# Optimization experiments

Measured on AMD Instinct MI355X. Metric: run time of the kernel, lower is better.

The kernel has to match this reference:

```python
import jax, jax.numpy as jnp
import numpy as np

NUM_HEADS = 16
EPS = 1e-5
BLOCK = 16  # score_mod: q_idx // 16 == kv_idx % 16


def _ln(x, eps=EPS):
    # LayerNorm, elementwise_affine=False
    m = jnp.mean(x, axis=-1, keepdims=True)
    v = jnp.mean((x - m) ** 2, axis=-1, keepdims=True)
    return (x - m) * jax.lax.rsqrt(v + eps)


def setup_inputs() -> dict:
    key = jax.random.key(0)
    ks = jax.random.split(key, 5)
    N, D = 2048, 2048
    w = 0.02
    return {
        "x": jax.random.normal(ks[0], (N, D), jnp.float32),
        "Wq": jax.random.normal(ks[1], (D, D), jnp.float32) * w,
        "Wk": jax.random.normal(ks[2], (D, D), jnp.float32) * w,
        "Wv": jax.random.normal(ks[3], (D, D), jnp.float32) * w,
        "Wo": jax.random.normal(ks[4], (D, D), jnp.float32) * w,
    }


def reference(x, Wq, Wk, Wv, Wo):
    N, D = x.shape
    H = NUM_HEADS
    DH = D // H
    x_in = x
    xn = _ln(x)
    # per-head q/k layernorm, cast to attention dtype (bfloat16)
    q = _ln((xn @ Wq).reshape(N, H, DH)).astype(jnp.bfloat16)
    k = _ln((xn @ Wk).reshape(N, H, DH)).astype(jnp.bfloat16)
    v = (xn @ Wv).reshape(N, H, DH)  # stays fp32 (original applies no cast to vs)
    scale = 1.0 / np.sqrt(DH)
    # dense scores then sparsity mask, as flex_attention with score_mod does
    scores = jnp.einsum("nhd,mhd->hnm", q, k, preferred_element_type=jnp.float32) * scale
    qi = jnp.arange(N)
    mask = (qi[:, None] // BLOCK) == (qi[None, :] % BLOCK)  # [N, N]
    s = jnp.where(mask[None, :, :], scores, -jnp.inf)
    # safe softmax: rows with no allowed keys (q_idx >= 256) produce zeros
    mx = jnp.max(s, axis=-1, keepdims=True)
    e = jnp.exp(s - jnp.where(jnp.isfinite(mx), mx, 0.0))
    denom = jnp.sum(e, axis=-1, keepdims=True)
    attn = e / jnp.maximum(denom, 1e-30)
    o = jnp.einsum("hnm,mhd->nhd", attn, v)  # [N, H, DH]
    out = o.reshape(N, D) @ Wo
    return out + x_in
```

## Files before the change

kernel.cpp:

```cpp
#include <hip/hip_runtime.h>

typedef unsigned short u16;
typedef __attribute__((ext_vector_type(8))) short short8;
typedef __attribute__((ext_vector_type(4))) float f32x4;

#define D 2048
#define EPS 1e-5f

__device__ __forceinline__ u16 f2bf(float f) {
  unsigned u = __float_as_uint(f);
  u += 0x7fffu + ((u >> 16) & 1u);
  return (u16)(u >> 16);
}

__device__ __forceinline__ void async16(const void* g, void* l) {
  __builtin_amdgcn_global_load_lds(
      (const __attribute__((address_space(1))) void*)g,
      (__attribute__((address_space(3))) void*)l, 16, 0, 0);
}

__global__ __launch_bounds__(256) void prep(const float* __restrict__ x,
                                            const float* __restrict__ Wq,
                                            const float* __restrict__ Wk,
                                            const float* __restrict__ Wv,
                                            const float* __restrict__ Wo,
                                            u16* __restrict__ xn,
                                            float* __restrict__ out,
                                            u16* __restrict__ WqT, u16* __restrict__ WkT,
                                            u16* __restrict__ WvT, u16* __restrict__ WoT) {
  int bid = blockIdx.x;
  int t = threadIdx.x;
  if (bid < 2048) {
    const float* xr = x + (size_t)bid * D;
    float4 v[2];
    float s = 0.f, sq = 0.f;
#pragma unroll
    for (int i = 0; i < 2; i++) {
      v[i] = *(const float4*)(xr + i * 1024 + t * 4);
      s += v[i].x + v[i].y + v[i].z + v[i].w;
      sq += v[i].x * v[i].x + v[i].y * v[i].y + v[i].z * v[i].z + v[i].w * v[i].w;
    }
#pragma unroll
    for (int m = 32; m >= 1; m >>= 1) { s += __shfl_xor(s, m); sq += __shfl_xor(sq, m); }
    __shared__ float ps[4], pq[4];
    int w = t >> 6, lane = t & 63;
    if (lane == 0) { ps[w] = s; pq[w] = sq; }
    __syncthreads();
    s = ps[0] + ps[1] + ps[2] + ps[3];
    sq = pq[0] + pq[1] + pq[2] + pq[3];
    float mean = s * (1.f / D);
    float var = sq * (1.f / D) - mean * mean;
    float rs = rsqrtf(var + EPS);
    float* outr = out + (size_t)bid * D;
    u16* xnr = xn + (size_t)bid * D;
#pragma unroll
    for (int i = 0; i < 2; i++) {
      *(float4*)(outr + i * 1024 + t * 4) = v[i];
      ushort4 o;
      o.x = f2bf((v[i].x - mean) * rs);
      o.y = f2bf((v[i].y - mean) * rs);
      o.z = f2bf((v[i].z - mean) * rs);
      o.w = f2bf((v[i].w - mean) * rs);
      *(ushort4*)(xnr + i * 1024 + t * 4) = o;
    }
  } else {
    int tb = bid - 2048;
    int wsel = tb >> 10;
    int tt = tb & 1023;
    const float* src; u16* dst;
    switch (wsel) {
      case 0: src = Wq; dst = WqT; break;
      case 1: src = Wk; dst = WkT; break;
      case 2: src = Wv; dst = WvT; break;
      default: src = Wo; dst = WoT; break;
    }
    int i0 = (tt >> 5) * 64, j0 = (tt & 31) * 64;
    __shared__ u16 tile[64 * 66];
#pragma unroll
    for (int r = 0; r < 4; r++) {
      int idx = r * 256 + t;
      int row = idx >> 4, c4 = idx & 15;
      float4 v = *(const float4*)(src + (size_t)(i0 + row) * D + j0 + c4 * 4);
      tile[row * 66 + c4 * 4 + 0] = f2bf(v.x);
      tile[row * 66 + c4 * 4 + 1] = f2bf(v.y);
      tile[row * 66 + c4 * 4 + 2] = f2bf(v.z);
      tile[row * 66 + c4 * 4 + 3] = f2bf(v.w);
    }
    __syncthreads();
#pragma unroll
    for (int r = 0; r < 4; r++) {
      int idx = r * 256 + t;
      int row = idx >> 4, c4 = idx & 15;
      ushort4 o;
      o.x = tile[(c4 * 4 + 0) * 66 + row];
      o.y = tile[(c4 * 4 + 1) * 66 + row];
      o.z = tile[(c4 * 4 + 2) * 66 + row];
      o.w = tile[(c4 * 4 + 3) * 66 + row];
      *(ushort4*)(dst + (size_t)(j0 + row) * D + i0 + c4 * 4) = o;
    }
  }
}

__device__ __forceinline__ void gemm_tile(const u16* __restrict__ A,
                                          const u16* __restrict__ Bt,
                                          bool permB, int m0, int n0,
                                          int kbeg, int kend,
                                          u16* As, u16* Bs, f32x4 acc[4][4]) {
  int tid = threadIdx.x, wid = tid >> 6, lane = tid & 63;
  int q4 = lane >> 4, m16 = lane & 15;
  int wm = wid >> 1, wn = wid & 1;
  for (int kb = kbeg; kb < kend; kb += 64) {
#pragma unroll
    for (int p = 0; p < 4; p++) {
      int idx = p * 256 + tid;
      int r = idx >> 3, sl = idx & 7;
      int gc = sl ^ (r & 7);
      async16(A + (size_t)(m0 + r) * D + kb + gc * 8, As + (size_t)(p * 256 + wid * 64) * 8);
      int rb = n0 + r;
      int gr = permB ? ((rb & 127) * 16 + (rb >> 7)) : rb;
      async16(Bt + (size_t)gr * D + kb + gc * 8, Bs + (size_t)(p * 256 + wid * 64) * 8);
    }
    __syncthreads();
#pragma unroll
    for (int ks = 0; ks < 2; ks++) {
      short8 af[4], bf[4];
      int c = ks * 4 + q4;
#pragma unroll
      for (int i = 0; i < 4; i++) {
        int ra = wm * 64 + i * 16 + m16;
        af[i] = *(const short8*)(As + ra * 64 + (c ^ (ra & 7)) * 8);
        int rb = wn * 64 + i * 16 + m16;
        bf[i] = *(const short8*)(Bs + rb * 64 + (c ^ (rb & 7)) * 8);
      }
#pragma unroll
      for (int i = 0; i < 4; i++)
#pragma unroll
        for (int j = 0; j < 4; j++)
          acc[i][j] = __builtin_amdgcn_mfma_f32_16x16x32_bf16(af[i], bf[j], acc[i][j], 0, 0, 0);
    }
    __syncthreads();
  }
}

__global__ __launch_bounds__(256, 3) void gemm_mega(const u16* __restrict__ xn,
                                                    const u16* __restrict__ WkT,
                                                    const u16* __restrict__ WvT,
                                                    const u16* __restrict__ WqT,
                                                    u16* __restrict__ K3,
                                                    u16* __restrict__ V3,
                                                    float* __restrict__ Qp) {
  __shared__ u16 smem[2 * 128 * 64];
  u16* As = smem;
  u16* Bs = smem + 8192;
  int bid0 = blockIdx.x;
  int tid = threadIdx.x, wid = tid >> 6, lane = tid & 63;
  int q4 = lane >> 4, m16 = lane & 15;
  int wm = wid >> 1, wn = wid & 1;

  if (bid0 >= 512) {
    int qb = bid0 - 512;
    int ks = qb & 7, t = qb >> 3;
    int m0 = (t >> 4) * 128, n0 = (t & 15) * 128;
    f32x4 acc[4][4];
#pragma unroll
    for (int i = 0; i < 4; i++)
#pragma unroll
      for (int j = 0; j < 4; j++)
#pragma unroll
        for (int r = 0; r < 4; r++) acc[i][j][r] = 0.f;
    gemm_tile(xn, WqT, false, m0, n0, ks * 256, ks * 256 + 256, As, Bs, acc);
    float* C = Qp + (size_t)ks * 256 * D;
#pragma unroll
    for (int i = 0; i < 4; i++)
#pragma unroll
      for (int j = 0; j < 4; j++)
#pragma unroll
        for (int r = 0; r < 4; r++) {
          int row = m0 + wm * 64 + i * 16 + q4 * 4 + r;
          int col = n0 + wn * 64 + j * 16 + m16;
          C[(size_t)row * D + col] = acc[i][j][r];
        }
    return;
  }

  int bid = (bid0 & 7) * 64 + (bid0 >> 3);
  int sel = bid >> 8;
  int z = bid & 255;
  int m0 = (z >> 4) * 128, n0 = (z & 15) * 128;
  const u16* A = sel ? WvT : xn;
  const u16* Bt = sel ? xn : WkT;
  f32x4 acc[4][4];
#pragma unroll
  for (int i = 0; i < 4; i++)
#pragma unroll
    for (int j = 0; j < 4; j++)
#pragma unroll
      for (int r = 0; r < 4; r++) acc[i][j][r] = 0.f;
  gemm_tile(A, Bt, sel == 1, m0, n0, 0, D, As, Bs, acc);

  if (sel == 1) {
    int h = m0 >> 7, b = n0 >> 7;
#pragma unroll
    for (int i = 0; i < 4; i++)
#pragma unroll
      for (int j = 0; j < 4; j++)
#pragma unroll
        for (int r = 0; r < 4; r++) {
          int dhl = wm * 64 + i * 16 + q4 * 4 + r;
          int key = wn * 64 + j * 16 + m16;
          V3[((size_t)(h * 16 + b) * 128 + dhl) * 128 + key] = f2bf(acc[i][j][r]);
        }
  } else {
    float* redS = (float*)smem;
    float* redQ = redS + 256;
    __syncthreads();
#pragma unroll
    for (int i = 0; i < 4; i++) {
      float ps[4], pq[4];
#pragma unroll
      for (int r = 0; r < 4; r++) {
        float s = 0.f, q = 0.f;
#pragma unroll
        for (int j = 0; j < 4; j++) { float a = acc[i][j][r]; s += a; q += a * a; }
#pragma unroll
        for (int msk = 1; msk < 16; msk <<= 1) {
          s += __shfl_xor(s, msk);
          q += __shfl_xor(q, msk);
        }
        ps[r] = s; pq[r] = q;
      }
      if (m16 == 0) {
#pragma unroll
        for (int r = 0; r < 4; r++) {
          int row = wm * 64 + i * 16 + q4 * 4 + r;
          redS[row * 2 + wn] = ps[r];
          redQ[row * 2 + wn] = pq[r];
        }
      }
    }
    __syncthreads();
    int h = n0 >> 7;
#pragma unroll
    for (int i = 0; i < 4; i++)
#pragma unroll
      for (int r = 0; r < 4; r++) {
        int row = wm * 64 + i * 16 + q4 * 4 + r;
        float S = redS[row * 2] + redS[row * 2 + 1];
        float Qs = redQ[row * 2] + redQ[row * 2 + 1];
        float mean = S * (1.f / 128.f);
        float var = Qs * (1.f / 128.f) - mean * mean;
        float rstd = rsqrtf(var + EPS);
        int tok = m0 + row;
#pragma unroll
        for (int j = 0; j < 4; j++) {
          int dhl = wn * 64 + j * 16 + m16;
          u16 val = f2bf((acc[i][j][r] - mean) * rstd);
          K3[(((size_t)(h * 16 + (tok & 15))) * 128 + (tok >> 4)) * 128 + dhl] = val;
        }
      }
  }
}

__global__ __launch_bounds__(256) void attn(const float* __restrict__ Qp,
                                            const u16* __restrict__ K3,
                                            const u16* __restrict__ V3,
                                            u16* __restrict__ Ob) {
  int bh = blockIdx.x;
  int h = bh & 15, b = bh >> 4;
  int tid = threadIdx.x, w = tid >> 6, lane = tid & 63;
  int q4 = lane >> 4, m16 = lane & 15;
  __shared__ u16 Qs[16][136];
  __shared__ u16 P[16][136];
  __shared__ float redmx[4][16];
  __shared__ float redsm[4][16];
  __shared__ float invd[16];
  const float scale = 0.08838834764831845f;
  const u16* Ktile = K3 + (size_t)(h * 16 + b) * 128 * 128;
  const u16* Vtile = V3 + (size_t)(h * 16 + b) * 128 * 128;

  {
    int row = tid >> 4;
    int c8 = (tid & 15) * 8;
    const float* qpb = Qp + (size_t)(b * 16 + row) * D + h * 128 + c8;
    float q8[8];
#pragma unroll
    for (int ii = 0; ii < 8; ii++) q8[ii] = 0.f;
#pragma unroll
    for (int ks = 0; ks < 8; ks++) {
      float4 a = *(const float4*)(qpb + (size_t)ks * 256 * D);
      float4 bb = *(const float4*)(qpb + (size_t)ks * 256 * D + 4);
      q8[0] += a.x; q8[1] += a.y; q8[2] += a.z; q8[3] += a.w;
      q8[4] += bb.x; q8[5] += bb.y; q8[6] += bb.z; q8[7] += bb.w;
    }
    float s = 0.f, sq = 0.f;
#pragma unroll
    for (int ii = 0; ii < 8; ii++) { s += q8[ii]; sq += q8[ii] * q8[ii]; }
#pragma unroll
    for (int msk = 1; msk < 16; msk <<= 1) { s += __shfl_xor(s, msk); sq += __shfl_xor(sq, msk); }
    float mean = s * (1.f / 128.f);
    float var = sq * (1.f / 128.f) - mean * mean;
    float rstd = rsqrtf(var + EPS);
#pragma unroll
    for (int ii = 0; ii < 8; ii++) Qs[row][c8 + ii] = f2bf((q8[ii] - mean) * rstd);
  }
  __syncthreads();

  short8 af[4];
#pragma unroll
  for (int dc = 0; dc < 4; dc++)
    af[dc] = *(const short8*)(&Qs[m16][dc * 32 + q4 * 8]);
  f32x4 s[2];
#pragma unroll
  for (int kt = 0; kt < 2; kt++)
#pragma unroll
    for (int r = 0; r < 4; r++) s[kt][r] = 0.f;
#pragma unroll
  for (int kt = 0; kt < 2; kt++) {
    int key = w * 32 + kt * 16 + m16;
#pragma unroll
    for (int dc = 0; dc < 4; dc++) {
      short8 bf = *(const short8*)(Ktile + (size_t)key * 128 + dc * 32 + q4 * 8);
      s[kt] = __builtin_amdgcn_mfma_f32_16x16x32_bf16(af[dc], bf, s[kt], 0, 0, 0);
    }
  }
  float mx[4];
#pragma unroll
  for (int r = 0; r < 4; r++) {
    mx[r] = fmaxf(s[0][r], s[1][r]);
#pragma unroll
    for (int msk = 1; msk < 16; msk <<= 1) mx[r] = fmaxf(mx[r], __shfl_xor(mx[r], msk));
    if (m16 == 0) redmx[w][q4 * 4 + r] = mx[r];
  }
  __syncthreads();
#pragma unroll
  for (int r = 0; r < 4; r++) {
    int row = q4 * 4 + r;
    float M = fmaxf(fmaxf(redmx[0][row], redmx[1][row]), fmaxf(redmx[2][row], redmx[3][row]));
    float acc = 0.f;
#pragma unroll
    for (int kt = 0; kt < 2; kt++) {
      float e = __expf((s[kt][r] - M) * scale);
      s[kt][r] = e;
      acc += e;
    }
#pragma unroll
    for (int msk = 1; msk < 16; msk <<= 1) acc += __shfl_xor(acc, msk);
    if (m16 == 0) redsm[w][row] = acc;
  }
#pragma unroll
  for (int kt = 0; kt < 2; kt++)
#pragma unroll
    for (int r = 0; r < 4; r++)
      P[q4 * 4 + r][w * 32 + kt * 16 + m16] = f2bf(s[kt][r]);
  __syncthreads();
  if (tid < 16) invd[tid] = 1.0f / (redsm[0][tid] + redsm[1][tid] + redsm[2][tid] + redsm[3][tid]);
  __syncthreads();

  short8 pf[4];
#pragma unroll
  for (int kc = 0; kc < 4; kc++)
    pf[kc] = *(const short8*)(&P[m16][kc * 32 + q4 * 8]);
  f32x4 o[2];
#pragma unroll
  for (int dt = 0; dt < 2; dt++)
#pragma unroll
    for (int r = 0; r < 4; r++) o[dt][r] = 0.f;
#pragma unroll
  for (int dt = 0; dt < 2; dt++) {
    int dhl = w * 32 + dt * 16 + m16;
#pragma unroll
    for (int kc = 0; kc < 4; kc++) {
      short8 vf = *(const short8*)(Vtile + (size_t)dhl * 128 + kc * 32 + q4 * 8);
      o[dt] = __builtin_amdgcn_mfma_f32_16x16x32_bf16(pf[kc], vf, o[dt], 0, 0, 0);
    }
  }
#pragma unroll
  for (int dt = 0; dt < 2; dt++)
#pragma unroll
    for (int r = 0; r < 4; r++) {
      int row = q4 * 4 + r;
      float val = o[dt][r] * invd[row];
      Ob[(size_t)(b * 16 + row) * D + h * 128 + w * 32 + dt * 16 + m16] = f2bf(val);
    }
}

__global__ __launch_bounds__(256, 3) void gemm_wo(const u16* __restrict__ Ob,
                                                  const u16* __restrict__ WoT,
                                                  float* __restrict__ Wpart) {
  __shared__ u16 smem[2 * 128 * 64];
  u16* As = smem;
  u16* Bs = smem + 8192;
  int m0 = blockIdx.x * 128, n0 = blockIdx.y * 128;
  int z = blockIdx.z;
  int k0 = z * 256;
  f32x4 acc[4][4];
#pragma unroll
  for (int i = 0; i < 4; i++)
#pragma unroll
    for (int j = 0; j < 4; j++)
#pragma unroll
      for (int r = 0; r < 4; r++) acc[i][j][r] = 0.f;
  gemm_tile(Ob, WoT, false, m0, n0, k0, k0 + 256, As, Bs, acc);
  float* C = Wpart + (size_t)z * 256 * D;
  int tid = threadIdx.x, wid = tid >> 6, lane = tid & 63;
  int q4 = lane >> 4, m16 = lane & 15;
  int wm = wid >> 1, wn = wid & 1;
#pragma unroll
  for (int i = 0; i < 4; i++)
#pragma unroll
    for (int j = 0; j < 4; j++)
#pragma unroll
      for (int r = 0; r < 4; r++) {
        int row = m0 + wm * 64 + i * 16 + q4 * 4 + r;
        int col = n0 + wn * 64 + j * 16 + m16;
        C[(size_t)row * D + col] = acc[i][j][r];
      }
}

__global__ __launch_bounds__(256) void reduce_wo(const float* __restrict__ Wpart,
                                                 float* __restrict__ out) {
  int i = (blockIdx.x * 256 + threadIdx.x) * 4;
  float4 s = *(const float4*)(out + i);
#pragma unroll
  for (int z = 0; z < 8; z++) {
    float4 p = *(const float4*)(Wpart + (size_t)z * 256 * D + i);
    s.x += p.x; s.y += p.y; s.z += p.z; s.w += p.w;
  }
  *(float4*)(out + i) = s;
}

extern "C" void kernel_launch(void* const* d_in, const int* in_sizes, int n_in,
                              void* d_out, int out_size, void* d_ws, size_t ws_size,
                              hipStream_t stream) {
  const float* x  = (const float*)d_in[0];
  const float* Wq = (const float*)d_in[1];
  const float* Wk = (const float*)d_in[2];
  const float* Wv = (const float*)d_in[3];
  const float* Wo = (const float*)d_in[4];
  float* out = (float*)d_out;
  char* w = (char*)d_ws;
  const size_t MB = 1u << 20;
  u16*   xn    = (u16*)(w);
  u16*   WqT   = (u16*)(w + 8 * MB);
  u16*   WkT   = (u16*)(w + 16 * MB);
  u16*   WvT   = (u16*)(w + 24 * MB);
  u16*   WoT   = (u16*)(w + 32 * MB);
  u16*   K3    = (u16*)(w + 40 * MB);
  u16*   V3    = (u16*)(w + 48 * MB);
  u16*   Obf   = (u16*)(w + 56 * MB);
  float* Qp    = (float*)(w + 58 * MB);
  float* Wpart = (float*)(w + 58 * MB);

  prep<<<dim3(6144), dim3(256), 0, stream>>>(x, Wq, Wk, Wv, Wo, xn, out, WqT, WkT, WvT, WoT);
  gemm_mega<<<dim3(768), dim3(256), 0, stream>>>(xn, WkT, WvT, WqT, K3, V3, Qp);
  attn<<<dim3(256), dim3(256), 0, stream>>>(Qp, K3, V3, Obf);
  gemm_wo<<<dim3(2, 16, 8), dim3(256), 0, stream>>>(Obf, WoT, Wpart);
  reduce_wo<<<dim3(512), dim3(256), 0, stream>>>(Wpart, out);
}
```

Measured before the change: 191.5 us.

## Fuse attention, Wo GEMM and reduction into one persistent kernel with grid barriers

Merges the attn, gemm_wo and reduce_wo launches into a single 256-block kernel, using atomic-counter grid barriers between phases. The barrier counters are reset inside the prep kernel. The aim is to remove two kernel launch gaps and their tail effects. In exchange, correctness depends on all 256 blocks being co-resident, the spin barriers add cost, and Qp and Wpart share workspace memory across phases that are now inside one kernel.

```diff
diff --git a/kernel.cpp b/kernel.cpp
--- a/kernel.cpp
+++ b/kernel.cpp
@@ -17,6 +17,18 @@
   __builtin_amdgcn_global_load_lds(
       (const __attribute__((address_space(1))) void*)g,
       (__attribute__((address_space(3))) void*)l, 16, 0, 0);
+}
+
+__device__ __forceinline__ void gridbar(unsigned* ctr) {
+  __syncthreads();
+  if (threadIdx.x == 0) {
+    __threadfence();
+    __hip_atomic_fetch_add(ctr, 1u, __ATOMIC_ACQ_REL, __HIP_MEMORY_SCOPE_AGENT);
+    while (__hip_atomic_load(ctr, __ATOMIC_ACQUIRE, __HIP_MEMORY_SCOPE_AGENT) < 256u)
+      __builtin_amdgcn_s_sleep(2);
+  }
+  __syncthreads();
+  __threadfence();
 }
 
 __global__ __launch_bounds__(256) void prep(const float* __restrict__ x,
@@ -27,9 +39,11 @@
                                             u16* __restrict__ xn,
                                             float* __restrict__ out,
                                             u16* __restrict__ WqT, u16* __restrict__ WkT,
-                                            u16* __restrict__ WvT, u16* __restrict__ WoT) {
+                                            u16* __restrict__ WvT, u16* __restrict__ WoT,
+                                            unsigned* __restrict__ bar) {
   int bid = blockIdx.x;
   int t = threadIdx.x;
+  if (bid == 2048 && t < 2) bar[t] = 0;
   if (bid < 2048) {
     const float* xr = x + (size_t)bid * D;
     float4 v[2];
@@ -261,172 +275,184 @@
   }
 }
 
-__global__ __launch_bounds__(256) void attn(const float* __restrict__ Qp,
-                                            const u16* __restrict__ K3,
-                                            const u16* __restrict__ V3,
-                                            u16* __restrict__ Ob) {
-  int bh = blockIdx.x;
-  int h = bh & 15, b = bh >> 4;
+__global__ __launch_bounds__(256, 2) void tail(const float* __restrict__ Qp,
+                                               const u16* __restrict__ K3,
+                                               const u16* __restrict__ V3,
+                                               const u16* __restrict__ WoT,
+                                               float* __restrict__ Wpart,
+                                               float* __restrict__ out,
+                                               u16* __restrict__ Ob,
+                                               unsigned* __restrict__ bar) {
+  __shared__ u16 smem[2 * 128 * 64];
+  int bid = blockIdx.x;
   int tid = threadIdx.x, w = tid >> 6, lane = tid & 63;
   int q4 = lane >> 4, m16 = lane & 15;
-  __shared__ u16 Qs[16][136];
-  __shared__ u16 P[16][136];
-  __shared__ float redmx[4][16];
-  __shared__ float redsm[4][16];
-  __shared__ float invd[16];
-  const float scale = 0.08838834764831845f;
-  const u16* Ktile = K3 + (size_t)(h * 16 + b) * 128 * 128;
-  const u16* Vtile = V3 + (size_t)(h * 16 + b) * 128 * 128;
 
   {
-    int row = tid >> 4;
-    int c8 = (tid & 15) * 8;
-    const float* qpb = Qp + (size_t)(b * 16 + row) * D + h * 128 + c8;
-    float q8[8];
-#pragma unroll
-    for (int ii = 0; ii < 8; ii++) q8[ii] = 0.f;
-#pragma unroll
-    for (int ks = 0; ks < 8; ks++) {
-      float4 a = *(const float4*)(qpb + (size_t)ks * 256 * D);
-      float4 bb = *(const float4*)(qpb + (size_t)ks * 256 * D + 4);
-      q8[0] += a.x; q8[1] += a.y; q8[2] += a.z; q8[3] += a.w;
-      q8[4] += bb.x; q8[5] += bb.y; q8[6] += bb.z; q8[7] += bb.w;
-    }
-    float s = 0.f, sq = 0.f;
-#pragma unroll
-    for (int ii = 0; ii < 8; ii++) { s += q8[ii]; sq += q8[ii] * q8[ii]; }
-#pragma unroll
-    for (int msk = 1; msk < 16; msk <<= 1) { s += __shfl_xor(s, msk); sq += __shfl_xor(sq, msk); }
-    float mean = s * (1.f / 128.f);
-    float var = sq * (1.f / 128.f) - mean * mean;
-    float rstd = rsqrtf(var + EPS);
-#pragma unroll
-    for (int ii = 0; ii < 8; ii++) Qs[row][c8 + ii] = f2bf((q8[ii] - mean) * rstd);
-  }
-  __syncthreads();
-
-  short8 af[4];
-#pragma unroll
-  for (int dc = 0; dc < 4; dc++)
-    af[dc] = *(const short8*)(&Qs[m16][dc * 32 + q4 * 8]);
-  f32x4 s[2];
-#pragma unroll
-  for (int kt = 0; kt < 2; kt++)
-#pragma unroll
-    for (int r = 0; r < 4; r++) s[kt][r] = 0.f;
-#pragma unroll
-  for (int kt = 0; kt < 2; kt++) {
-    int key = w * 32 + kt * 16 + m16;
-#pragma unroll
-    for (int dc = 0; dc < 4; dc++) {
-      short8 bf = *(const short8*)(Ktile + (size_t)key * 128 + dc * 32 + q4 * 8);
-      s[kt] = __builtin_amdgcn_mfma_f32_16x16x32_bf16(af[dc], bf, s[kt], 0, 0, 0);
-    }
-  }
-  float mx[4];
-#pragma unroll
-  for (int r = 0; r < 4; r++) {
-    mx[r] = fmaxf(s[0][r], s[1][r]);
-#pragma unroll
-    for (int msk = 1; msk < 16; msk <<= 1) mx[r] = fmaxf(mx[r], __shfl_xor(mx[r], msk));
-    if (m16 == 0) redmx[w][q4 * 4 + r] = mx[r];
-  }
-  __syncthreads();
-#pragma unroll
-  for (int r = 0; r < 4; r++) {
-    int row = q4 * 4 + r;
-    float M = fmaxf(fmaxf(redmx[0][row], redmx[1][row]), fmaxf(redmx[2][row], redmx[3][row]));
-    float acc = 0.f;
+    int h = bid & 15, b = bid >> 4;
+    u16* Qs = smem;
+    u16* P  = smem + 16 * 136;
+    float* redmx = (float*)(smem + 2 * 16 * 136);
+    float* redsm = redmx + 64;
+    float* invd  = redsm + 64;
+    const float scale = 0.08838834764831845f;
+    const u16* Ktile = K3 + (size_t)(h * 16 + b) * 128 * 128;
+    const u16* Vtile = V3 + (size_t)(h * 16 + b) * 128 * 128;
+
+    {
+      int row = tid >> 4;
+      int c8 = (tid & 15) * 8;
+      const float* qpb = Qp + (size_t)(b * 16 + row) * D + h * 128 + c8;
+      float q8[8];
+#pragma unroll
+      for (int ii = 0; ii < 8; ii++) q8[ii] = 0.f;
+#pragma unroll
+      for (int ks = 0; ks < 8; ks++) {
+        float4 a = *(const float4*)(qpb + (size_t)ks * 256 * D);
+        float4 bb = *(const float4*)(qpb + (size_t)ks * 256 * D + 4);
+        q8[0] += a.x; q8[1] += a.y; q8[2] += a.z; q8[3] += a.w;
+        q8[4] += bb.x; q8[5] += bb.y; q8[6] += bb.z; q8[7] += bb.w;
+      }
+      float s = 0.f, sq = 0.f;
+#pragma unroll
+      for (int ii = 0; ii < 8; ii++) { s += q8[ii]; sq += q8[ii] * q8[ii]; }
+#pragma unroll
+      for (int msk = 1; msk < 16; msk <<= 1) { s += __shfl_xor(s, msk); sq += __shfl_xor(sq, msk); }
+      float mean = s * (1.f / 128.f);
+      float var = sq * (1.f / 128.f) - mean * mean;
+      float rstd = rsqrtf(var + EPS);
+#pragma unroll
+      for (int ii = 0; ii < 8; ii++) Qs[row * 136 + c8 + ii] = f2bf((q8[ii] - mean) * rstd);
+    }
+    __syncthreads();
+
+    short8 af[4];
+#pragma unroll
+    for (int dc = 0; dc < 4; dc++)
+      af[dc] = *(const short8*)(&Qs[m16 * 136 + dc * 32 + q4 * 8]);
+    f32x4 s[2];
+#pragma unroll
+    for (int kt = 0; kt < 2; kt++)
+#pragma unroll
+      for (int r = 0; r < 4; r++) s[kt][r] = 0.f;
 #pragma unroll
     for (int kt = 0; kt < 2; kt++) {
-      float e = __expf((s[kt][r] - M) * scale);
-      s[kt][r] = e;
-      acc += e;
-    }
-#pragma unroll
-    for (int msk = 1; msk < 16; msk <<= 1) acc += __shfl_xor(acc, msk);
-    if (m16 == 0) redsm[w][row] = acc;
-  }
-#pragma unroll
-  for (int kt = 0; kt < 2; kt++)
-#pragma unroll
-    for (int r = 0; r < 4; r++)
-      P[q4 * 4 + r][w * 32 + kt * 16 + m16] = f2bf(s[kt][r]);
-  __syncthreads();
-  if (tid < 16) invd[tid] = 1.0f / (redsm[0][tid] + redsm[1][tid] + redsm[2][tid] + redsm[3][tid]);
-  __syncthreads();
-
-  short8 pf[4];
-#pragma unroll
-  for (int kc = 0; kc < 4; kc++)
-    pf[kc] = *(const short8*)(&P[m16][kc * 32 + q4 * 8]);
-  f32x4 o[2];
-#pragma unroll
-  for (int dt = 0; dt < 2; dt++)
-#pragma unroll
-    for (int r = 0; r < 4; r++) o[dt][r] = 0.f;
-#pragma unroll
-  for (int dt = 0; dt < 2; dt++) {
-    int dhl = w * 32 + dt * 16 + m16;
-#pragma unroll
-    for (int kc = 0; kc < 4; kc++) {
-      short8 vf = *(const short8*)(Vtile + (size_t)dhl * 128 + kc * 32 + q4 * 8);
-      o[dt] = __builtin_amdgcn_mfma_f32_16x16x32_bf16(pf[kc], vf, o[dt], 0, 0, 0);
-    }
-  }
-#pragma unroll
-  for (int dt = 0; dt < 2; dt++)
+      int key = w * 32 + kt * 16 + m16;
+#pragma unroll
+      for (int dc = 0; dc < 4; dc++) {
+        short8 bf = *(const short8*)(Ktile + (size_t)key * 128 + dc * 32 + q4 * 8);
+        s[kt] = __builtin_amdgcn_mfma_f32_16x16x32_bf16(af[dc], bf, s[kt], 0, 0, 0);
+      }
+    }
+    float mx[4];
+#pragma unroll
+    for (int r = 0; r < 4; r++) {
+      mx[r] = fmaxf(s[0][r], s[1][r]);
+#pragma unroll
+      for (int msk = 1; msk < 16; msk <<= 1) mx[r] = fmaxf(mx[r], __shfl_xor(mx[r], msk));
+      if (m16 == 0) redmx[w * 16 + q4 * 4 + r] = mx[r];
+    }
+    __syncthreads();
 #pragma unroll
     for (int r = 0; r < 4; r++) {
       int row = q4 * 4 + r;
-      float val = o[dt][r] * invd[row];
-      Ob[(size_t)(b * 16 + row) * D + h * 128 + w * 32 + dt * 16 + m16] = f2bf(val);
-    }
-}
-
-__global__ __launch_bounds__(256, 3) void gemm_wo(const u16* __restrict__ Ob,
-                                                  const u16* __restrict__ WoT,
-                                                  float* __restrict__ Wpart) {
-  __shared__ u16 smem[2 * 128 * 64];
-  u16* As = smem;
-  u16* Bs = smem + 8192;
-  int m0 = blockIdx.x * 128, n0 = blockIdx.y * 128;
-  int z = blockIdx.z;
-  int k0 = z * 256;
-  f32x4 acc[4][4];
-#pragma unroll
-  for (int i = 0; i < 4; i++)
-#pragma unroll
-    for (int j = 0; j < 4; j++)
-#pragma unroll
-      for (int r = 0; r < 4; r++) acc[i][j][r] = 0.f;
-  gemm_tile(Ob, WoT, false, m0, n0, k0, k0 + 256, As, Bs, acc);
-  float* C = Wpart + (size_t)z * 256 * D;
-  int tid = threadIdx.x, wid = tid >> 6, lane = tid & 63;
-  int q4 = lane >> 4, m16 = lane & 15;
-  int wm = wid >> 1, wn = wid & 1;
-#pragma unroll
-  for (int i = 0; i < 4; i++)
-#pragma unroll
-    for (int j = 0; j < 4; j++)
+      float M = fmaxf(fmaxf(redmx[row], redmx[16 + row]), fmaxf(redmx[32 + row], redmx[48 + row]));
+      float acc = 0.f;
+#pragma unroll
+      for (int kt = 0; kt < 2; kt++) {
+        float e = __expf((s[kt][r] - M) * scale);
+        s[kt][r] = e;
+        acc += e;
+      }
+#pragma unroll
+      for (int msk = 1; msk < 16; msk <<= 1) acc += __shfl_xor(acc, msk);
+      if (m16 == 0) redsm[w * 16 + row] = acc;
+    }
+#pragma unroll
+    for (int kt = 0; kt < 2; kt++)
+#pragma unroll
+      for (int r = 0; r < 4; r++)
+        P[(q4 * 4 + r) * 136 + w * 32 + kt * 16 + m16] = f2bf(s[kt][r]);
+    __syncthreads();
+    if (tid < 16) invd[tid] = 1.0f / (redsm[tid] + redsm[16 + tid] + redsm[32 + tid] + redsm[48 + tid]);
+    __syncthreads();
+
+    short8 pf[4];
+#pragma unroll
+    for (int kc = 0; kc < 4; kc++)
+      pf[kc] = *(const short8*)(&P[m16 * 136 + kc * 32 + q4 * 8]);
+    f32x4 o[2];
+#pragma unroll
+    for (int dt = 0; dt < 2; dt++)
+#pragma unroll
+      for (int r = 0; r < 4; r++) o[dt][r] = 0.f;
+#pragma unroll
+    for (int dt = 0; dt < 2; dt++) {
+      int dhl = w * 32 + dt * 16 + m16;
+#pragma unroll
+      for (int kc = 0; kc < 4; kc++) {
+        short8 vf = *(const short8*)(Vtile + (size_t)dhl * 128 + kc * 32 + q4 * 8);
+        o[dt] = __builtin_amdgcn_mfma_f32_16x16x32_bf16(pf[kc], vf, o[dt], 0, 0, 0);
+      }
+    }
+#pragma unroll
+    for (int dt = 0; dt < 2; dt++)
 #pragma unroll
       for (int r = 0; r < 4; r++) {
-        int row = m0 + wm * 64 + i * 16 + q4 * 4 + r;
-        int col = n0 + wn * 64 + j * 16 + m16;
-        C[(size_t)row * D + col] = acc[i][j][r];
-      }
-}
-
-__global__ __launch_bounds__(256) void reduce_wo(const float* __restrict__ Wpart,
-                                                 float* __restrict__ out) {
-  int i = (blockIdx.x * 256 + threadIdx.x) * 4;
-  float4 s = *(const float4*)(out + i);
-#pragma unroll
-  for (int z = 0; z < 8; z++) {
-    float4 p = *(const float4*)(Wpart + (size_t)z * 256 * D + i);
-    s.x += p.x; s.y += p.y; s.z += p.z; s.w += p.w;
-  }
-  *(float4*)(out + i) = s;
+        int row = q4 * 4 + r;
+        float val = o[dt][r] * invd[row];
+        Ob[(size_t)(b * 16 + row) * D + h * 128 + w * 32 + dt * 16 + m16] = f2bf(val);
+      }
+  }
+
+  gridbar(bar + 0);
+
+  {
+    u16* As = smem;
+    u16* Bs = smem + 8192;
+    int m0 = (bid >> 7) * 128;
+    int n0 = ((bid >> 3) & 15) * 128;
+    int z = bid & 7;
+    int k0 = z * 256;
+    f32x4 acc[4][4];
+#pragma unroll
+    for (int i = 0; i < 4; i++)
+#pragma unroll
+      for (int j = 0; j < 4; j++)
+#pragma unroll
+        for (int r = 0; r < 4; r++) acc[i][j][r] = 0.f;
+    gemm_tile(Ob, WoT, false, m0, n0, k0, k0 + 256, As, Bs, acc);
+    float* C = Wpart + (size_t)z * 256 * D;
+    int wid = tid >> 6;
+    int wm = wid >> 1, wn = wid & 1;
+#pragma unroll
+    for (int i = 0; i < 4; i++)
+#pragma unroll
+      for (int j = 0; j < 4; j++)
+#pragma unroll
+        for (int r = 0; r < 4; r++) {
+          int row = m0 + wm * 64 + i * 16 + q4 * 4 + r;
+          int col = n0 + wn * 64 + j * 16 + m16;
+          C[(size_t)row * D + col] = acc[i][j][r];
+        }
+  }
+
+  gridbar(bar + 1);
+
+  {
+    int i0 = (bid * 256 + tid) * 8;
+#pragma unroll
+    for (int half = 0; half < 2; half++) {
+      int i = i0 + half * 4;
+      float4 s = *(const float4*)(out + i);
+#pragma unroll
+      for (int z = 0; z < 8; z++) {
+        float4 p = *(const float4*)(Wpart + (size_t)z * 256 * D + i);
+        s.x += p.x; s.y += p.y; s.z += p.z; s.w += p.w;
+      }
+      *(float4*)(out + i) = s;
+    }
+  }
 }
 
 extern "C" void kernel_launch(void* const* d_in, const int* in_sizes, int n_in,
@@ -448,12 +474,11 @@
   u16*   K3    = (u16*)(w + 40 * MB);
   u16*   V3    = (u16*)(w + 48 * MB);
   u16*   Obf   = (u16*)(w + 56 * MB);
+  unsigned* bar = (unsigned*)(w + 57 * MB);
   float* Qp    = (float*)(w + 58 * MB);
   float* Wpart = (float*)(w + 58 * MB);
 
-  prep<<<dim3(6144), dim3(256), 0, stream>>>(x, Wq, Wk, Wv, Wo, xn, out, WqT, WkT, WvT, WoT);
+  prep<<<dim3(6144), dim3(256), 0, stream>>>(x, Wq, Wk, Wv, Wo, xn, out, WqT, WkT, WvT, WoT, bar);
   gemm_mega<<<dim3(768), dim3(256), 0, stream>>>(xn, WkT, WvT, WqT, K3, V3, Qp);
-  attn<<<dim3(256), dim3(256), 0, stream>>>(Qp, K3, V3, Obf);
-  gemm_wo<<<dim3(2, 16, 8), dim3(256), 0, stream>>>(Obf, WoT, Wpart);
-  reduce_wo<<<dim3(512), dim3(256), 0, stream>>>(Wpart, out);
-}
+  tail<<<dim3(256), dim3(256), 0, stream>>>(Qp, K3, V3, WoT, Wpart, out, Obf, bar);
+}
```

New measurement: 274.7 us. 1.43x slower.
